# Performance work log

Measured on AMD Instinct MI355X. Metric: run time of the kernel, lower is better.

The kernel has to match this reference:

```python
import jax, jax.numpy as jnp
import numpy as np

N, D, H, C, M = 100000, 128, 4, 32, 3  # nodes, dim, heads, head_dim, metapaths
E = 400000  # edges per metapath


def setup_inputs() -> dict:
    key = jax.random.key(0)
    ks = jax.random.split(key, 12)
    inp = {
        'x_l': jax.random.normal(ks[0], (N, D), jnp.float32),
        'x_r': jax.random.normal(ks[1], (N, D), jnp.float32),
        'edge_index': jax.random.randint(ks[2], (M, 2, E), 0, N, jnp.int64),
        # linear_l / linear_r per node type (single 'gene' type)
        'Wl': jax.random.normal(ks[3], (D, D), jnp.float32) * 0.05,
        'bl': jnp.zeros((D,), jnp.float32),
        'Wr': jax.random.normal(ks[4], (D, D), jnp.float32) * 0.05,
        'br': jnp.zeros((D,), jnp.float32),
        # Conv1d(in=D, out=M+1, kernel=1) == dense [M+1, D] + bias
        'Wc': jax.random.normal(ks[5], (M + 1, D), jnp.float32) * 0.05,
        'bc': jnp.zeros((M + 1,), jnp.float32),
        'attn_l': jax.random.normal(ks[6], (M, H, C), jnp.float32) * 0.1,
        'attn_r': jax.random.normal(ks[7], (M, H, C), jnp.float32) * 0.1,
        'sharpen': jnp.ones((M,), jnp.float32),  # attn_activation='sharpening'
    }
    return inp


def reference(x_l, x_r, Wl, bl, Wr, br, Wc, bc, attn_l, attn_r, sharpen, edge_index):
    n = x_l.shape[0]
    l = (x_l @ Wl.T + bl).reshape(n, H, C)  # left projection  [N,H,C]
    r = (x_r @ Wr.T + br).reshape(n, H, C)  # right projection [N,H,C]
    # relation-mixing weights beta via 1x1 conv + softmax over relations
    beta = jax.nn.softmax(x_l @ Wc.T + bc, axis=1)  # [N, M+1]

    def agg(edges, al_m, ar_m, s_m):
        idx, nbr = edges[0], edges[1]  # aggregation index (i), neighbor (j)
        # per-edge, per-channel attention logits (alpha_j + alpha_i), sharpened
        a = (l[nbr] * al_m + r[idx] * ar_m) * s_m  # [E,H,C]
        # edge softmax segmented over destination node
        amax = jax.ops.segment_max(a, idx, num_segments=n)
        ex = jnp.exp(a - amax[idx])
        den = jax.ops.segment_sum(ex, idx, num_segments=n)
        att = ex / (den[idx] + 1e-16)
        # message = x_j * alpha, scatter-add aggregation
        return jax.ops.segment_sum(l[nbr] * att, idx, num_segments=n).reshape(n, D)

    rel = [agg(edge_index[m], attn_l[m], attn_r[m], sharpen[m]) for m in range(M)]
    rel.append(l.reshape(n, D))  # last relation slot = self (left) embedding
    emb = jnp.stack(rel, axis=1)  # [N, M+1, D]
    out = jnp.einsum('nrd,nr->nd', emb, beta)  # bmm(emb^T, beta).squeeze
    return jax.nn.relu(out)
```

## Files before the change

kernel.cpp:

```cpp
#include <hip/hip_runtime.h>
#include <math.h>

#define NN 100000
#define DD 128
#define MM 3
#define EE 400000
#define CAP 32


__global__ void k_detect(const int* __restrict__ ei, int* __restrict__ flag) {
  if (threadIdx.x == 0 && blockIdx.x == 0) {
    int orsum = 0;
    for (int i = 0; i < 64; ++i) orsum |= ei[2 * i + 1];
    flag[0] = (orsum == 0) ? 1 : 0;
  }
}

__global__ __launch_bounds__(256, 2)
void k_prep(const float* __restrict__ x,
            const float* __restrict__ Wl,
            const float* __restrict__ bl,
            const float* __restrict__ Wc,
            const float* __restrict__ bc,
            float* __restrict__ l_out,
            float* __restrict__ beta_out,
            int* __restrict__ deg) {
  __shared__ float xs[64][132];
  __shared__ float wlt[64][130];
  __shared__ float wcs[4][132];
  __shared__ float bcs[4];
  const int t = threadIdx.x;
  const int r0 = blockIdx.x * 64;

  #pragma unroll
  for (int i = 0; i < 8; ++i) {
    int f4 = t + 256 * i;
    int row = f4 >> 5;
    int kq = f4 & 31;
    int gr = r0 + row; if (gr >= NN) gr = NN - 1;
    float4 v = *reinterpret_cast<const float4*>(&x[(size_t)gr * DD + kq * 4]);
    *reinterpret_cast<float4*>(&xs[row][kq * 4]) = v;
  }
  if (t < 128) {
    int m = t >> 5, kq = t & 31;
    float4 v = *reinterpret_cast<const float4*>(&Wc[m * DD + kq * 4]);
    *reinterpret_cast<float4*>(&wcs[m][kq * 4]) = v;
  }
  if (t < 4) bcs[t] = bc[t];
  if (t < 192) {
    int m = t >> 6;
    int n = r0 + (t & 63);
    if (n < NN) deg[m * NN + n] = 0;
  }

  const int w = t >> 6;
  const int lane = t & 63;
  float acc0[16], acc1[16];
  #pragma unroll
  for (int r = 0; r < 16; ++r) { acc0[r] = 0.f; acc1[r] = 0.f; }

  for (int h = 0; h < 2; ++h) {
    __syncthreads();
    #pragma unroll
    for (int i = 0; i < 8; ++i) {
      int f4 = t + 256 * i;
      int j = f4 >> 4;
      int kq = f4 & 15;
      float4 v = *reinterpret_cast<const float4*>(&Wl[j * DD + h * 64 + kq * 4]);
      wlt[kq * 4 + 0][j] = v.x;
      wlt[kq * 4 + 1][j] = v.y;
      wlt[kq * 4 + 2][j] = v.z;
      wlt[kq * 4 + 3][j] = v.w;
    }
    __syncthreads();
    #pragma unroll
    for (int kq = 0; kq < 16; ++kq) {
      float2 w0 = *reinterpret_cast<const float2*>(&wlt[kq * 4 + 0][lane * 2]);
      float2 w1 = *reinterpret_cast<const float2*>(&wlt[kq * 4 + 1][lane * 2]);
      float2 w2 = *reinterpret_cast<const float2*>(&wlt[kq * 4 + 2][lane * 2]);
      float2 w3 = *reinterpret_cast<const float2*>(&wlt[kq * 4 + 3][lane * 2]);
      #pragma unroll
      for (int r = 0; r < 16; ++r) {
        float4 xv = *reinterpret_cast<const float4*>(&xs[w * 16 + r][h * 64 + kq * 4]);
        acc0[r] += xv.x * w0.x; acc0[r] += xv.y * w1.x;
        acc0[r] += xv.z * w2.x; acc0[r] += xv.w * w3.x;
        acc1[r] += xv.x * w0.y; acc1[r] += xv.y * w1.y;
        acc1[r] += xv.z * w2.y; acc1[r] += xv.w * w3.y;
      }
    }
  }

  float2 blv = *reinterpret_cast<const float2*>(&bl[lane * 2]);
  #pragma unroll
  for (int r = 0; r < 16; ++r) {
    int row = r0 + w * 16 + r;
    if (row < NN) {
      float2 o; o.x = acc0[r] + blv.x; o.y = acc1[r] + blv.y;
      *reinterpret_cast<float2*>(&l_out[(size_t)row * DD + lane * 2]) = o;
    }
  }

  {
    int r = t >> 2, m = t & 3;
    float lg = bcs[m];
    for (int k = 0; k < 128; ++k) lg += xs[r][k] * wcs[m][k];
    float mx = fmaxf(lg, __shfl_xor(lg, 1, 4));
    mx = fmaxf(mx, __shfl_xor(mx, 2, 4));
    float e = __expf(lg - mx);
    float s = e + __shfl_xor(e, 1, 4);
    s += __shfl_xor(s, 2, 4);
    int n = r0 + r;
    if (n < NN) beta_out[n * 4 + m] = e / s;
  }
}

__global__ __launch_bounds__(256)
void k_scatter(const int* __restrict__ ei, const int* __restrict__ flag,
               int* __restrict__ deg, int* __restrict__ lst) {
  int i = blockIdx.x * 256 + threadIdx.x;
  if (i >= MM * EE) return;
  int m = i / EE, e = i - m * EE;
  size_t pi = (size_t)m * 2 * EE + e;
  size_t pn = pi + EE;
  int idx, nbr;
  if (flag[0]) { idx = ei[2 * pi]; nbr = ei[2 * pn]; }
  else         { idx = ei[pi];     nbr = ei[pn];     }
  int slot = atomicAdd(&deg[m * NN + idx], 1);
  if (slot < CAP) lst[((size_t)m * NN + idx) * CAP + slot] = nbr;
}

__global__ __launch_bounds__(256, 8)
void k_agg(const float* __restrict__ l, const float* __restrict__ beta,
           const int* __restrict__ deg, const int* __restrict__ lst,
           const float* __restrict__ attn_l, const float* __restrict__ sharpen,
           float* __restrict__ out) {
  const int lane = threadIdx.x & 63;
  const int node = blockIdx.x * 4 + (threadIdx.x >> 6);
  if (node >= NN) return;
  const int ch0 = lane * 2;

  float2 ls = *reinterpret_cast<const float2*>(&l[(size_t)node * DD + ch0]);
  float4 bt = *reinterpret_cast<const float4*>(&beta[(size_t)node * 4]);
  float acc0 = bt.w * ls.x;
  float acc1 = bt.w * ls.y;

  #pragma unroll 1
  for (int m = 0; m < MM; ++m) {
    float sm = sharpen[m];
    float2 al = *reinterpret_cast<const float2*>(&attn_l[m * DD + ch0]);
    al.x *= sm; al.y *= sm;

    int cnt = deg[m * NN + node];
    if (cnt > CAP) cnt = CAP;

    float num0 = 0.f, num1 = 0.f, den0 = 0.f, den1 = 0.f;
    if (cnt > 0) {
      const int* lb = lst + ((size_t)m * NN + node) * CAP;
      int nbr_reg = (lane < cnt) ? lb[lane] : 0;

      for (int s0 = 0; s0 < cnt; s0 += 8) {
        int ub = cnt - s0; if (ub > 8) ub = 8;
        float2 v[8];
        #pragma unroll
        for (int k = 0; k < 8; ++k) {
          int ss = s0 + k; if (ss >= cnt) ss = cnt - 1;
          int nb = __builtin_amdgcn_readlane(nbr_reg, ss);
          v[k] = *reinterpret_cast<const float2*>(&l[(size_t)nb * DD + ch0]);
        }
        #pragma unroll
        for (int k = 0; k < 8; ++k) {
          if (k < ub) {
            float e0 = __expf(v[k].x * al.x);
            float e1 = __expf(v[k].y * al.y);
            den0 += e0;            den1 += e1;
            num0 += v[k].x * e0;   num1 += v[k].y * e1;
          }
        }
      }
    }
    float bm = (m == 0) ? bt.x : (m == 1) ? bt.y : bt.z;
    acc0 += bm * (num0 / (den0 + 1e-16f));
    acc1 += bm * (num1 / (den1 + 1e-16f));
  }

  float2 o;
  o.x = fmaxf(acc0, 0.f);
  o.y = fmaxf(acc1, 0.f);
  *reinterpret_cast<float2*>(&out[(size_t)node * DD + ch0]) = o;
}

extern "C" void kernel_launch(void* const* d_in, const int* in_sizes, int n_in,
                              void* d_out, int out_size, void* d_ws, size_t ws_size,
                              hipStream_t stream) {
  const float* x_l     = (const float*)d_in[0];
  const int*   ei      = (const int*)d_in[2];
  const float* Wl      = (const float*)d_in[3];
  const float* bl      = (const float*)d_in[4];
  const float* Wc      = (const float*)d_in[7];
  const float* bc      = (const float*)d_in[8];
  const float* attn_l  = (const float*)d_in[9];
  const float* sharpen = (const float*)d_in[11];
  float* out = (float*)d_out;

  float* l    = (float*)d_ws;
  float* beta = l + (size_t)NN * DD;
  int*   deg  = (int*)(beta + (size_t)NN * 4);
  int*   lst  = deg + (size_t)MM * NN;
  int*   flag = lst + (size_t)MM * NN * CAP;

  k_detect<<<1, 64, 0, stream>>>(ei, flag);
  k_prep<<<(NN + 63) / 64, 256, 0, stream>>>(x_l, Wl, bl, Wc, bc, l, beta, deg);
  k_scatter<<<(MM * EE + 255) / 256, 256, 0, stream>>>(ei, flag, deg, lst);
  k_agg<<<(NN * 64 + 255) / 256, 256, 0, stream>>>(l, beta, deg, lst, attn_l, sharpen, out);
}
```

Before: 415.0 us.

## Aggregate with 32 lanes per node using float4 gathers and hoisted metapath loads

```diff
diff --git a/kernel.cpp b/kernel.cpp
--- a/kernel.cpp
+++ b/kernel.cpp
@@ -129,64 +129,88 @@
   if (slot < CAP) lst[((size_t)m * NN + idx) * CAP + slot] = nbr;
 }
 
-__global__ __launch_bounds__(256, 8)
+__global__ __launch_bounds__(256, 4)
 void k_agg(const float* __restrict__ l, const float* __restrict__ beta,
            const int* __restrict__ deg, const int* __restrict__ lst,
            const float* __restrict__ attn_l, const float* __restrict__ sharpen,
            float* __restrict__ out) {
-  const int lane = threadIdx.x & 63;
-  const int node = blockIdx.x * 4 + (threadIdx.x >> 6);
+  int tid = blockIdx.x * 256 + threadIdx.x;
+  int node = tid >> 5;
   if (node >= NN) return;
-  const int ch0 = lane * 2;
-
-  float2 ls = *reinterpret_cast<const float2*>(&l[(size_t)node * DD + ch0]);
-  float4 bt = *reinterpret_cast<const float4*>(&beta[(size_t)node * 4]);
-  float acc0 = bt.w * ls.x;
-  float acc1 = bt.w * ls.y;
-
-  #pragma unroll 1
-  for (int m = 0; m < MM; ++m) {
-    float sm = sharpen[m];
-    float2 al = *reinterpret_cast<const float2*>(&attn_l[m * DD + ch0]);
-    al.x *= sm; al.y *= sm;
-
-    int cnt = deg[m * NN + node];
-    if (cnt > CAP) cnt = CAP;
-
-    float num0 = 0.f, num1 = 0.f, den0 = 0.f, den1 = 0.f;
-    if (cnt > 0) {
-      const int* lb = lst + ((size_t)m * NN + node) * CAP;
-      int nbr_reg = (lane < cnt) ? lb[lane] : 0;
-
-      for (int s0 = 0; s0 < cnt; s0 += 8) {
-        int ub = cnt - s0; if (ub > 8) ub = 8;
-        float2 v[8];
-        #pragma unroll
-        for (int k = 0; k < 8; ++k) {
-          int ss = s0 + k; if (ss >= cnt) ss = cnt - 1;
-          int nb = __builtin_amdgcn_readlane(nbr_reg, ss);
-          v[k] = *reinterpret_cast<const float2*>(&l[(size_t)nb * DD + ch0]);
-        }
-        #pragma unroll
-        for (int k = 0; k < 8; ++k) {
-          if (k < ub) {
-            float e0 = __expf(v[k].x * al.x);
-            float e1 = __expf(v[k].y * al.y);
-            den0 += e0;            den1 += e1;
-            num0 += v[k].x * e0;   num1 += v[k].y * e1;
-          }
-        }
-      }
-    }
-    float bm = (m == 0) ? bt.x : (m == 1) ? bt.y : bt.z;
-    acc0 += bm * (num0 / (den0 + 1e-16f));
-    acc1 += bm * (num1 / (den1 + 1e-16f));
-  }
-
-  float2 o;
+  int ch0 = (tid & 31) << 2;
+
+  float4 ls  = *reinterpret_cast<const float4*>(&l[(size_t)node * DD + ch0]);
+  float4 bt  = *reinterpret_cast<const float4*>(&beta[(size_t)node * 4]);
+  int c0 = deg[node];
+  int c1 = deg[NN + node];
+  int c2 = deg[2 * NN + node];
+  float s0 = sharpen[0], s1 = sharpen[1], s2 = sharpen[2];
+  float4 av0 = *reinterpret_cast<const float4*>(&attn_l[0 * DD + ch0]);
+  float4 av1 = *reinterpret_cast<const float4*>(&attn_l[1 * DD + ch0]);
+  float4 av2 = *reinterpret_cast<const float4*>(&attn_l[2 * DD + ch0]);
+  c0 = min(c0, CAP); c1 = min(c1, CAP); c2 = min(c2, CAP);
+  av0.x *= s0; av0.y *= s0; av0.z *= s0; av0.w *= s0;
+  av1.x *= s1; av1.y *= s1; av1.z *= s1; av1.w *= s1;
+  av2.x *= s2; av2.y *= s2; av2.z *= s2; av2.w *= s2;
+
+  float acc0 = bt.w * ls.x, acc1 = bt.w * ls.y,
+        acc2 = bt.w * ls.z, acc3 = bt.w * ls.w;
+
+  const int* lb0 = lst + (size_t)node * CAP;
+  const int* lb1 = lst + ((size_t)NN + node) * CAP;
+  const int* lb2 = lst + ((size_t)(2 * NN) + node) * CAP;
+
+  auto do_m = [&](int cm, const int* lbm, float4 alv, float bm) {
+    float n0 = 0.f, n1 = 0.f, n2 = 0.f, n3 = 0.f;
+    float d0 = 0.f, d1 = 0.f, d2 = 0.f, d3 = 0.f;
+    int4 ia, ib;
+    if (cm > 0) ia = *reinterpret_cast<const int4*>(lbm);
+    if (cm > 4) ib = *reinterpret_cast<const int4*>(lbm + 4);
+    float4 v0, v1, v2, v3, v4, v5, v6, v7;
+    if (cm > 0) v0 = *reinterpret_cast<const float4*>(&l[(size_t)ia.x * DD + ch0]);
+    if (cm > 1) v1 = *reinterpret_cast<const float4*>(&l[(size_t)ia.y * DD + ch0]);
+    if (cm > 2) v2 = *reinterpret_cast<const float4*>(&l[(size_t)ia.z * DD + ch0]);
+    if (cm > 3) v3 = *reinterpret_cast<const float4*>(&l[(size_t)ia.w * DD + ch0]);
+    if (cm > 4) v4 = *reinterpret_cast<const float4*>(&l[(size_t)ib.x * DD + ch0]);
+    if (cm > 5) v5 = *reinterpret_cast<const float4*>(&l[(size_t)ib.y * DD + ch0]);
+    if (cm > 6) v6 = *reinterpret_cast<const float4*>(&l[(size_t)ib.z * DD + ch0]);
+    if (cm > 7) v7 = *reinterpret_cast<const float4*>(&l[(size_t)ib.w * DD + ch0]);
+#define CONSUME(K, V) \
+    if (cm > K) { \
+      float e; \
+      e = __expf(V.x * alv.x); d0 += e; n0 += V.x * e; \
+      e = __expf(V.y * alv.y); d1 += e; n1 += V.y * e; \
+      e = __expf(V.z * alv.z); d2 += e; n2 += V.z * e; \
+      e = __expf(V.w * alv.w); d3 += e; n3 += V.w * e; \
+    }
+    CONSUME(0, v0) CONSUME(1, v1) CONSUME(2, v2) CONSUME(3, v3)
+    CONSUME(4, v4) CONSUME(5, v5) CONSUME(6, v6) CONSUME(7, v7)
+#undef CONSUME
+    for (int s = 8; s < cm; ++s) {
+      int nb = lbm[s];
+      float4 vv = *reinterpret_cast<const float4*>(&l[(size_t)nb * DD + ch0]);
+      float e;
+      e = __expf(vv.x * alv.x); d0 += e; n0 += vv.x * e;
+      e = __expf(vv.y * alv.y); d1 += e; n1 += vv.y * e;
+      e = __expf(vv.z * alv.z); d2 += e; n2 += vv.z * e;
+      e = __expf(vv.w * alv.w); d3 += e; n3 += vv.w * e;
+    }
+    acc0 += bm * (n0 / (d0 + 1e-16f));
+    acc1 += bm * (n1 / (d1 + 1e-16f));
+    acc2 += bm * (n2 / (d2 + 1e-16f));
+    acc3 += bm * (n3 / (d3 + 1e-16f));
+  };
+
+  do_m(c0, lb0, av0, bt.x);
+  do_m(c1, lb1, av1, bt.y);
+  do_m(c2, lb2, av2, bt.z);
+
+  float4 o;
   o.x = fmaxf(acc0, 0.f);
   o.y = fmaxf(acc1, 0.f);
-  *reinterpret_cast<float2*>(&out[(size_t)node * DD + ch0]) = o;
+  o.z = fmaxf(acc2, 0.f);
+  o.w = fmaxf(acc3, 0.f);
+  *reinterpret_cast<float4*>(&out[(size_t)node * DD + ch0]) = o;
 }
 
 extern "C" void kernel_launch(void* const* d_in, const int* in_sizes, int n_in,
@@ -211,5 +235,5 @@
   k_detect<<<1, 64, 0, stream>>>(ei, flag);
   k_prep<<<(NN + 63) / 64, 256, 0, stream>>>(x_l, Wl, bl, Wc, bc, l, beta, deg);
   k_scatter<<<(MM * EE + 255) / 256, 256, 0, stream>>>(ei, flag, deg, lst);
-  k_agg<<<(NN * 64 + 255) / 256, 256, 0, stream>>>(l, beta, deg, lst, attn_l, sharpen, out);
-}
+  k_agg<<<(NN * 32 + 255) / 256, 256, 0, stream>>>(l, beta, deg, lst, attn_l, sharpen, out);
+}
```

Measured after the change: 379.7 us. 8.5% less time.
